# Optimization experiments

Measured on AMD Instinct MI355X. Metric: run time of the kernel, lower is better.

The kernel has to match this reference:

```python
import jax, jax.numpy as jnp
import numpy as np

N = 50000   # nodes
E = 600000  # edges per relation
H = 4       # heads
DH = 32     # head dim (out_feat // num_heads)
D = 128     # in_feat == out_feat
NEG_SLOPE = 0.2


def setup_inputs() -> dict:
    key = jax.random.key(0)
    ks = jax.random.split(key, 13)
    x = jax.random.normal(ks[0], (N, D), jnp.float32)
    src_r0 = jax.random.randint(ks[1], (E,), 0, N, jnp.int32)
    dst_r0 = jax.random.randint(ks[2], (E,), 0, N, jnp.int32)
    src_r1 = jax.random.randint(ks[3], (E,), 0, N, jnp.int32)
    dst_r1 = jax.random.randint(ks[4], (E,), 0, N, jnp.int32)
    s = 0.05  # keep activations moderate (xavier-like scale)
    W_r0 = jax.random.normal(ks[5], (D, H * DH), jnp.float32) * s
    attn_l_r0 = jax.random.normal(ks[6], (H, DH), jnp.float32) * s
    attn_r_r0 = jax.random.normal(ks[7], (H, DH), jnp.float32) * s
    W_r1 = jax.random.normal(ks[8], (D, H * DH), jnp.float32) * s
    attn_l_r1 = jax.random.normal(ks[9], (H, DH), jnp.float32) * s
    attn_r_r1 = jax.random.normal(ks[10], (H, DH), jnp.float32) * s
    loop_weight = jax.random.normal(ks[11], (D, D), jnp.float32) * s
    h_bias = jnp.zeros((D,), jnp.float32)
    return {"x": x, "src_r0": src_r0, "dst_r0": dst_r0, "src_r1": src_r1,
            "dst_r1": dst_r1, "W_r0": W_r0, "attn_l_r0": attn_l_r0,
            "attn_r_r0": attn_r_r0, "W_r1": W_r1, "attn_l_r1": attn_l_r1,
            "attn_r_r1": attn_r_r1, "loop_weight": loop_weight, "h_bias": h_bias}


def _gat_rel(x, src, dst, W, attn_l, attn_r):
    """DGL GATConv for one relation: fc -> per-node attn scalars -> edge
    leaky_relu -> per-dst softmax -> weighted scatter-sum. Heads flattened."""
    feat = (x @ W).reshape(-1, H, DH)                 # [N, H, DH]
    el = jnp.einsum('nhd,hd->nh', feat, attn_l)       # [N, H]
    er = jnp.einsum('nhd,hd->nh', feat, attn_r)       # [N, H]
    e = jax.nn.leaky_relu(el[src] + er[dst], NEG_SLOPE)  # [E, H]
    # edge softmax per destination node, per head (numerically stable)
    m = jax.ops.segment_max(e, dst, num_segments=N)   # [N, H]
    ex = jnp.exp(e - m[dst])                          # [E, H]
    z = jax.ops.segment_sum(ex, dst, num_segments=N)  # [N, H]
    a = ex / z[dst]                                   # [E, H]
    msg = a[:, :, None] * feat[src]                   # [E, H, DH]
    out = jax.ops.segment_sum(msg, dst, num_segments=N)  # [N, H, DH]
    return out.reshape(-1, H * DH)                    # [N, D] (concat heads)


def reference(x, src_r0, dst_r0, src_r1, dst_r1, W_r0, attn_l_r0, attn_r_r0,
              W_r1, attn_l_r1, attn_r_r1, loop_weight, h_bias):
    # HeteroGraphConv with default 'sum' aggregation across relations
    h = _gat_rel(x, src_r0, dst_r0, W_r0, attn_l_r0, attn_r_r0)
    h = h + _gat_rel(x, src_r1, dst_r1, W_r1, attn_l_r1, attn_r_r1)
    # self-loop linear + bias + activation (dropout p=0.0 is identity)
    h = h + x @ loop_weight + h_bias
    return jax.nn.relu(h)
```

## Files before the change

kernel.cpp:

```cpp
#include <hip/hip_runtime.h>
#include <math.h>


#define CAP 48
#define NB 256
#define BCAP 2752
#define BIN_EDGES 4096

typedef __attribute__((ext_vector_type(8))) short short8v;
typedef __attribute__((ext_vector_type(4))) float float4v;

__device__ __forceinline__ unsigned short f2bf(float f) {
  unsigned int u = __float_as_uint(f);
  unsigned int r = (u + 0x7fffu + ((u >> 16) & 1u)) >> 16;
  return (unsigned short)r;
}
__device__ __forceinline__ float2 bfpair(unsigned int u) {
  float2 r;
  r.x = __uint_as_float(u << 16);
  r.y = __uint_as_float(u & 0xffff0000u);
  return r;
}

__global__ __launch_bounds__(512) void prep_bin_kernel(
    const float* __restrict__ W0, const float* __restrict__ W1,
    const float* __restrict__ WL,
    const float* __restrict__ al0, const float* __restrict__ ar0,
    const float* __restrict__ al1, const float* __restrict__ ar1,
    const int* __restrict__ src0, const int* __restrict__ dst0,
    const int* __restrict__ src1, const int* __restrict__ dst1,
    unsigned short* __restrict__ Wtall,
    unsigned int* __restrict__ bpair, int* __restrict__ gcnt,
    int E, int width, int nconvb, int nbin)
{
  __shared__ int smem[512];
  const int t = threadIdx.x;

  if ((int)blockIdx.x < nconvb) {
    const int j = blockIdx.x * 512 + t;
    if (j < 4096) {
      const int rel = j >> 11;
      const int q = j & 2047;
      const int n = q >> 4;
      const int k0 = (q & 15) * 8;
      const float* W = rel ? W1 : W0;
      unsigned short o[8];
#pragma unroll
      for (int u = 0; u < 8; ++u) o[u] = f2bf(W[(size_t)(k0 + u) * 128 + n]);
      *(short8v*)&Wtall[(size_t)rel * 18432 + n * 128 + k0] = *(short8v*)o;
    } else if (j < 4352) {
      const int e = j - 4096;
      const int rel = e >> 7;
      const int q = e & 127;
      const int cIdx = q >> 4;
      const int isr = cIdx >> 2;
      const int h = cIdx & 3;
      const int k0 = (q & 15) * 8;
      const float* W = rel ? W1 : W0;
      const float* av = isr ? (rel ? ar1 : ar0) : (rel ? al1 : al0);
      unsigned short o[8];
#pragma unroll
      for (int u = 0; u < 8; ++u) {
        float s = 0.f;
#pragma unroll
        for (int d = 0; d < 32; ++d)
          s += W[(size_t)(k0 + u) * 128 + h * 32 + d] * av[h * 32 + d];
        o[u] = f2bf(s);
      }
      *(short8v*)&Wtall[(size_t)rel * 18432 + (128 + cIdx) * 128 + k0] = *(short8v*)o;
    } else if (j < 4608) {
      const int e = j - 4352;
      const int rel = e >> 7;
      const int q = e & 127;
      const int cIdx = 136 + (q >> 4);
      const int k0 = (q & 15) * 8;
      const short8v z = {0,0,0,0,0,0,0,0};
      *(short8v*)&Wtall[(size_t)rel * 18432 + cIdx * 128 + k0] = z;
    } else if (j < 6656) {
      const int e = j - 4608;
      const int n = e >> 4;
      const int k0 = (e & 15) * 8;
      unsigned short o[8];
#pragma unroll
      for (int u = 0; u < 8; ++u) o[u] = f2bf(WL[(size_t)(k0 + u) * 128 + n]);
      *(short8v*)&Wtall[(size_t)2 * 18432 + n * 128 + k0] = *(short8v*)o;
    }
  } else {
    int* cnt = smem;
    int* gb  = smem + NB;
    const int bid = blockIdx.x - nconvb;
    const int rel = (bid >= nbin) ? 1 : 0;
    const int ib  = rel ? (bid - nbin) : bid;
    const int* srcA = rel ? src1 : src0;
    const int* dstA = rel ? dst1 : dst0;
    const int base = ib * BIN_EDGES;
    const int cntE = min(E - base, BIN_EDGES);

    for (int i = t; i < NB; i += 512) cnt[i] = 0;
    __syncthreads();

    unsigned int epack[8]; int eb[8], epos[8];
#pragma unroll
    for (int q = 0; q < 8; ++q) {
      const int ei = t * 8 + q;
      if (ei < cntE) {
        const int s = srcA[base + ei];
        const int d = dstA[base + ei];
        const int b = d / width;
        const int ld = d - b * width;
        epack[q] = (unsigned int)s | ((unsigned int)ld << 16);
        eb[q] = b;
        epos[q] = atomicAdd(&cnt[b], 1);
      } else {
        eb[q] = -1;
      }
    }
    __syncthreads();
    for (int i = t; i < NB; i += 512)
      gb[i] = atomicAdd(&gcnt[rel * NB + i], cnt[i]);
    __syncthreads();
#pragma unroll
    for (int q = 0; q < 8; ++q) {
      if (eb[q] >= 0) {
        const int slot = gb[eb[q]] + epos[q];
        if (slot < BCAP)
          bpair[(size_t)(rel * NB + eb[q]) * BCAP + slot] = epack[q];
      }
    }
  }
}

__global__ __launch_bounds__(256) void gemm_ell_kernel(
    const float* __restrict__ x, const unsigned short* __restrict__ Wtall,
    unsigned short* __restrict__ f0, unsigned short* __restrict__ f1,
    unsigned short* __restrict__ xl,
    float* __restrict__ el0, float* __restrict__ er0,
    float* __restrict__ el1, float* __restrict__ er1,
    const unsigned int* __restrict__ bpair, const int* __restrict__ gcnt,
    int* __restrict__ deg, unsigned short* __restrict__ ell0,
    unsigned short* __restrict__ ell1,
    int N, int width, int ngemm)
{
  __shared__ int ldeg[256];

  if ((int)blockIdx.x < ngemm) {
    const int wave = threadIdx.x >> 6, lane = threadIdx.x & 63;
    const int lr = lane & 15, lk = lane >> 4;
    const int row0 = blockIdx.x * 64 + wave * 16;
    const int r = row0 + lr;

    short8v a[4];
#pragma unroll
    for (int kc = 0; kc < 4; ++kc) {
      if (r < N) {
        const float* xp = &x[(size_t)r * 128 + kc * 32 + lk * 8];
        float4 u = *(const float4*)xp;
        float4 v = *(const float4*)(xp + 4);
        unsigned short o[8];
        o[0]=f2bf(u.x); o[1]=f2bf(u.y); o[2]=f2bf(u.z); o[3]=f2bf(u.w);
        o[4]=f2bf(v.x); o[5]=f2bf(v.y); o[6]=f2bf(v.z); o[7]=f2bf(v.w);
        a[kc] = *(short8v*)o;
      } else {
        a[kc] = (short8v){0,0,0,0,0,0,0,0};
      }
    }

#pragma unroll
    for (int w = 0; w < 3; ++w) {
      const unsigned short* Wp = Wtall + (size_t)w * 18432;
      const int NF = (w < 2) ? 9 : 8;
      float4v acc[9];
#pragma unroll
      for (int nf = 0; nf < 9; ++nf) acc[nf] = (float4v){0.f, 0.f, 0.f, 0.f};
      for (int nf = 0; nf < NF; ++nf) {
        const unsigned short* Bp = &Wp[(size_t)(nf * 16 + lr) * 128];
#pragma unroll
        for (int kc = 0; kc < 4; ++kc) {
          const short8v b = *(const short8v*)&Bp[kc * 32 + lk * 8];
          acc[nf] = __builtin_amdgcn_mfma_f32_16x16x32_bf16(a[kc], b, acc[nf], 0, 0, 0);
        }
      }

      unsigned short* dstp = (w == 0) ? f0 : (w == 1) ? f1 : xl;
#pragma unroll
      for (int nf = 0; nf < 8; ++nf) {
        const int col = nf * 16 + lr;
#pragma unroll
        for (int j = 0; j < 4; ++j) {
          const int row = row0 + lk * 4 + j;
          if (row < N) dstp[(size_t)row * 128 + col] = f2bf(acc[nf][j]);
        }
      }
      if (w < 2 && lr < 8) {
        float* ep = (lr < 4) ? (w ? el1 : el0) : (w ? er1 : er0);
        const int h = lr & 3;
#pragma unroll
        for (int j = 0; j < 4; ++j) {
          const int row = row0 + lk * 4 + j;
          if (row < N) ep[row * 4 + h] = acc[8][j];
        }
      }
    }
  } else {
    const int bid = blockIdx.x - ngemm;
    const int rel = bid >> 8;
    const int b = bid & 255;
    const int t = threadIdx.x;
    const int d0 = b * width;
    if (t < width) ldeg[t] = 0;
    __syncthreads();
    const int count = min(gcnt[rel * NB + b], BCAP);
    unsigned short* ell = rel ? ell1 : ell0;
    const unsigned int* bp = &bpair[(size_t)(rel * NB + b) * BCAP];
    for (int i = t; i < count; i += 256) {
      const unsigned int v = bp[i];
      const int src = (int)(v & 0xFFFFu);
      const int ld = (int)(v >> 16);
      const int slot = atomicAdd(&ldeg[ld], 1);
      if (slot < CAP) ell[(size_t)(d0 + ld) * CAP + slot] = (unsigned short)src;
    }
    __syncthreads();
    if (t < width && d0 + t < N) deg[rel * N + d0 + t] = ldeg[t];
  }
}

__global__ __launch_bounds__(256) void gat_aggregate_kernel(
    const unsigned short* __restrict__ f0, const unsigned short* __restrict__ f1,
    const unsigned short* __restrict__ xl,
    const float* __restrict__ el0, const float* __restrict__ er0,
    const float* __restrict__ el1, const float* __restrict__ er1,
    const int* __restrict__ deg,
    const unsigned short* __restrict__ ell0, const unsigned short* __restrict__ ell1,
    const float* __restrict__ bias, float* __restrict__ out, int N)
{
  __shared__ float p_lds[4][2][4][16];
  const int wid  = threadIdx.x >> 6;
  const int lane = threadIdx.x & 63;
  const int n = blockIdx.x * 4 + wid;
  if (n >= N) return;
  const int h  = lane >> 4;
  const int il = lane & 15;
  const int c  = lane * 2;

  const int rs0 = (int)ell0[(size_t)n * CAP + il];
  const int rs1 = (int)ell1[(size_t)n * CAP + il];
  const int d0 = min(deg[n], CAP);
  const int d1 = min(deg[N + n], CAP);
  const float er0h = er0[n * 4 + h];
  const float er1h = er1[n * 4 + h];

  const bool v0 = il < d0, v1 = il < d1;
  const int s0 = v0 ? rs0 : 0;
  const int s1 = v1 ? rs1 : 0;
  const float elv0 = el0[s0 * 4 + h];
  const float elv1 = el1[s1 * 4 + h];

  float m0, sum0, m1, sum1;
  {
    float e = elv0 + er0h;  e = e > 0.f ? e : 0.2f * e;
    float ev = v0 ? e : -INFINITY;
    float cm = ev;
    cm = fmaxf(cm, __shfl_xor(cm, 1)); cm = fmaxf(cm, __shfl_xor(cm, 2));
    cm = fmaxf(cm, __shfl_xor(cm, 4)); cm = fmaxf(cm, __shfl_xor(cm, 8));
    const float p = __expf(ev - cm);
    float cs = p;
    cs += __shfl_xor(cs, 1); cs += __shfl_xor(cs, 2);
    cs += __shfl_xor(cs, 4); cs += __shfl_xor(cs, 8);
    m0 = cm; sum0 = cs;
    p_lds[wid][0][h][il] = p;
  }
  {
    float e = elv1 + er1h;  e = e > 0.f ? e : 0.2f * e;
    float ev = v1 ? e : -INFINITY;
    float cm = ev;
    cm = fmaxf(cm, __shfl_xor(cm, 1)); cm = fmaxf(cm, __shfl_xor(cm, 2));
    cm = fmaxf(cm, __shfl_xor(cm, 4)); cm = fmaxf(cm, __shfl_xor(cm, 8));
    const float p = __expf(ev - cm);
    float cs = p;
    cs += __shfl_xor(cs, 1); cs += __shfl_xor(cs, 2);
    cs += __shfl_xor(cs, 4); cs += __shfl_xor(cs, 8);
    m1 = cm; sum1 = cs;
    p_lds[wid][1][h][il] = p;
  }

  unsigned int fu0[16], fu1[16];
#pragma unroll
  for (int i = 0; i < 16; ++i) {
    const int s = __builtin_amdgcn_readlane(s0, i);
    fu0[i] = *(const unsigned int*)&f0[(size_t)s * 128 + c];
  }
#pragma unroll
  for (int i = 0; i < 16; ++i) {
    const int s = __builtin_amdgcn_readlane(s1, i);
    fu1[i] = *(const unsigned int*)&f1[(size_t)s * 128 + c];
  }

  float ax0 = 0.f, ay0 = 0.f;
  {
    float p16[16];
    *(float4*)&p16[0]  = *(const float4*)&p_lds[wid][0][h][0];
    *(float4*)&p16[4]  = *(const float4*)&p_lds[wid][0][h][4];
    *(float4*)&p16[8]  = *(const float4*)&p_lds[wid][0][h][8];
    *(float4*)&p16[12] = *(const float4*)&p_lds[wid][0][h][12];
    float axa=0.f, aya=0.f, axb=0.f, ayb=0.f;
#pragma unroll
    for (int i = 0; i < 16; i += 2) {
      const float2 fa = bfpair(fu0[i]);
      const float2 fb2 = bfpair(fu0[i+1]);
      axa += p16[i]*fa.x;   aya += p16[i]*fa.y;
      axb += p16[i+1]*fb2.x; ayb += p16[i+1]*fb2.y;
    }
    ax0 = axa + axb; ay0 = aya + ayb;
  }
  float ax1 = 0.f, ay1 = 0.f;
  {
    float p16[16];
    *(float4*)&p16[0]  = *(const float4*)&p_lds[wid][1][h][0];
    *(float4*)&p16[4]  = *(const float4*)&p_lds[wid][1][h][4];
    *(float4*)&p16[8]  = *(const float4*)&p_lds[wid][1][h][8];
    *(float4*)&p16[12] = *(const float4*)&p_lds[wid][1][h][12];
    float axa=0.f, aya=0.f, axb=0.f, ayb=0.f;
#pragma unroll
    for (int i = 0; i < 16; i += 2) {
      const float2 fa = bfpair(fu1[i]);
      const float2 fb2 = bfpair(fu1[i+1]);
      axa += p16[i]*fa.x;   aya += p16[i]*fa.y;
      axb += p16[i+1]*fb2.x; ayb += p16[i+1]*fb2.y;
    }
    ax1 = axa + axb; ay1 = aya + ayb;
  }

  auto tail = [&](const unsigned short* ellp, const float* elp, float erh,
                  int d, const unsigned short* fbp, float& m, float& sum,
                  float& ax, float& ay, int slot) {
    for (int base = 16; base < d; base += 16) {
      const bool valid = (base + il) < d;
      int sv = (int)ellp[(size_t)n * CAP + base + il];
      sv = valid ? sv : 0;
      const float elv = elp[sv * 4 + h];
      float e = elv + erh; e = e > 0.f ? e : 0.2f * e;
      const float ev = valid ? e : -INFINITY;
      float cm = ev;
      cm = fmaxf(cm, __shfl_xor(cm, 1)); cm = fmaxf(cm, __shfl_xor(cm, 2));
      cm = fmaxf(cm, __shfl_xor(cm, 4)); cm = fmaxf(cm, __shfl_xor(cm, 8));
      const float mn = fmaxf(m, cm);
      const float scale = __expf(m - mn);
      const float p = __expf(ev - mn);
      float cs = p;
      cs += __shfl_xor(cs, 1); cs += __shfl_xor(cs, 2);
      cs += __shfl_xor(cs, 4); cs += __shfl_xor(cs, 8);
      sum = sum * scale + cs;
      m = mn;
      p_lds[wid][slot][h][il] = p;
      unsigned int fu[16];
#pragma unroll
      for (int i = 0; i < 16; ++i) {
        const int s = __builtin_amdgcn_readlane(sv, i);
        fu[i] = *(const unsigned int*)&fbp[(size_t)s * 128 + c];
      }
      float p16[16];
      *(float4*)&p16[0]  = *(const float4*)&p_lds[wid][slot][h][0];
      *(float4*)&p16[4]  = *(const float4*)&p_lds[wid][slot][h][4];
      *(float4*)&p16[8]  = *(const float4*)&p_lds[wid][slot][h][8];
      *(float4*)&p16[12] = *(const float4*)&p_lds[wid][slot][h][12];
      float axa=0.f, aya=0.f;
#pragma unroll
      for (int i = 0; i < 16; ++i) {
        const float2 f = bfpair(fu[i]);
        axa += p16[i]*f.x; aya += p16[i]*f.y;
      }
      ax = ax * scale + axa;
      ay = ay * scale + aya;
    }
  };
  if (d0 > 16) tail(ell0, el0, er0h, d0, f0, m0, sum0, ax0, ay0, 0);
  if (d1 > 16) tail(ell1, el1, er1h, d1, f1, m1, sum1, ax1, ay1, 1);

  float ox = 0.f, oy = 0.f;
  if (d0 > 0) { const float inv = 1.f / sum0; ox += ax0 * inv; oy += ay0 * inv; }
  if (d1 > 0) { const float inv = 1.f / sum1; ox += ax1 * inv; oy += ay1 * inv; }
  const float2 xlv = bfpair(*(const unsigned int*)&xl[(size_t)n * 128 + c]);
  const float2 bv  = *(const float2*)&bias[c];
  ox += xlv.x + bv.x;
  oy += xlv.y + bv.y;
  float2 res;
  res.x = fmaxf(ox, 0.f);
  res.y = fmaxf(oy, 0.f);
  *(float2*)&out[(size_t)n * 128 + c] = res;
}

extern "C" void kernel_launch(void* const* d_in, const int* in_sizes, int n_in,
                              void* d_out, int out_size, void* d_ws, size_t ws_size,
                              hipStream_t stream)
{
  const int N = in_sizes[0] / 128;
  const int E = in_sizes[1];

  const float* x    = (const float*)d_in[0];
  const int* src0   = (const int*)d_in[1];
  const int* dst0   = (const int*)d_in[2];
  const int* src1   = (const int*)d_in[3];
  const int* dst1   = (const int*)d_in[4];
  const float* W0   = (const float*)d_in[5];
  const float* al0  = (const float*)d_in[6];
  const float* ar0  = (const float*)d_in[7];
  const float* W1   = (const float*)d_in[8];
  const float* al1  = (const float*)d_in[9];
  const float* ar1  = (const float*)d_in[10];
  const float* WL   = (const float*)d_in[11];
  const float* bias = (const float*)d_in[12];
  float* out = (float*)d_out;

  char* p = (char*)d_ws;
  auto alloc = [&](size_t bytes) { char* r = p; p += (bytes + 255) & ~(size_t)255; return r; };
  unsigned short* f0 = (unsigned short*)alloc((size_t)N * 128 * 2);
  unsigned short* f1 = (unsigned short*)alloc((size_t)N * 128 * 2);
  unsigned short* xl = (unsigned short*)alloc((size_t)N * 128 * 2);
  float* el0 = (float*)alloc((size_t)N * 4 * 4);
  float* er0 = (float*)alloc((size_t)N * 4 * 4);
  float* el1 = (float*)alloc((size_t)N * 4 * 4);
  float* er1 = (float*)alloc((size_t)N * 4 * 4);
  int* deg   = (int*)alloc((size_t)2 * N * 4);
  unsigned short* ell0 = (unsigned short*)alloc((size_t)CAP * N * 2);
  unsigned short* ell1 = (unsigned short*)alloc((size_t)CAP * N * 2);
  unsigned int* bpair = (unsigned int*)alloc((size_t)2 * NB * BCAP * 4);
  int* gcnt  = (int*)alloc((size_t)2 * NB * 4);
  unsigned short* Wtall = (unsigned short*)alloc((size_t)(2 * 144 + 128) * 128 * 2);

  const int width = (N + NB - 1) / NB;
  const int ngemm = (N + 63) / 64;
  const int nbin  = (E + BIN_EDGES - 1) / BIN_EDGES;
  const int nconvb = 13;

  hipMemsetAsync(gcnt, 0, (size_t)2 * NB * 4, stream);

  prep_bin_kernel<<<nconvb + 2 * nbin, 512, 0, stream>>>(
      W0, W1, WL, al0, ar0, al1, ar1, src0, dst0, src1, dst1,
      Wtall, bpair, gcnt, E, width, nconvb, nbin);

  gemm_ell_kernel<<<ngemm + 2 * NB, 256, 0, stream>>>(
      x, Wtall, f0, f1, xl, el0, er0, el1, er1,
      bpair, gcnt, deg, ell0, ell1, N, width, ngemm);

  gat_aggregate_kernel<<<(N + 3) / 4, 256, 0, stream>>>(
      f0, f1, xl, el0, er0, el1, er1, deg, ell0, ell1, bias, out, N);
}
```

Measured before the change: 153.4 us.

## Process more work per thread across binning, GEMM, and aggregation kernels

The binning stage now handles 8192 edges per block, with 16 edges per thread in a strided coalesced layout. The GEMM computes two 16-row M fragments per wave, so each B-fragment load feeds two MFMAs. The aggregation kernel processes two destination nodes per wave so more independent gathers are in flight. The cost is higher register pressure and fewer blocks, which may reduce occupancy.

```diff
diff --git a/kernel.cpp b/kernel.cpp
--- a/kernel.cpp
+++ b/kernel.cpp
@@ -5,7 +5,7 @@
 #define CAP 48
 #define NB 256
 #define BCAP 2752
-#define BIN_EDGES 4096
+#define BIN_EDGES 8192
 
 typedef __attribute__((ext_vector_type(8))) short short8v;
 typedef __attribute__((ext_vector_type(4))) float float4v;
@@ -99,10 +99,10 @@
     for (int i = t; i < NB; i += 512) cnt[i] = 0;
     __syncthreads();
 
-    unsigned int epack[8]; int eb[8], epos[8];
-#pragma unroll
-    for (int q = 0; q < 8; ++q) {
-      const int ei = t * 8 + q;
+    unsigned int epack[16]; int eb[16], epos[16];
+#pragma unroll
+    for (int q = 0; q < 16; ++q) {
+      const int ei = q * 512 + t;
       if (ei < cntE) {
         const int s = srcA[base + ei];
         const int d = dstA[base + ei];
@@ -120,7 +120,7 @@
       gb[i] = atomicAdd(&gcnt[rel * NB + i], cnt[i]);
     __syncthreads();
 #pragma unroll
-    for (int q = 0; q < 8; ++q) {
+    for (int q = 0; q < 16; ++q) {
       if (eb[q] >= 0) {
         const int slot = gb[eb[q]] + epos[q];
         if (slot < BCAP)
@@ -146,22 +146,25 @@
   if ((int)blockIdx.x < ngemm) {
     const int wave = threadIdx.x >> 6, lane = threadIdx.x & 63;
     const int lr = lane & 15, lk = lane >> 4;
-    const int row0 = blockIdx.x * 64 + wave * 16;
-    const int r = row0 + lr;
-
-    short8v a[4];
-#pragma unroll
-    for (int kc = 0; kc < 4; ++kc) {
-      if (r < N) {
-        const float* xp = &x[(size_t)r * 128 + kc * 32 + lk * 8];
-        float4 u = *(const float4*)xp;
-        float4 v = *(const float4*)(xp + 4);
-        unsigned short o[8];
-        o[0]=f2bf(u.x); o[1]=f2bf(u.y); o[2]=f2bf(u.z); o[3]=f2bf(u.w);
-        o[4]=f2bf(v.x); o[5]=f2bf(v.y); o[6]=f2bf(v.z); o[7]=f2bf(v.w);
-        a[kc] = *(short8v*)o;
-      } else {
-        a[kc] = (short8v){0,0,0,0,0,0,0,0};
+    const int row0 = blockIdx.x * 128 + wave * 32;
+
+    short8v a[2][4];
+#pragma unroll
+    for (int mf = 0; mf < 2; ++mf) {
+      const int r = row0 + mf * 16 + lr;
+#pragma unroll
+      for (int kc = 0; kc < 4; ++kc) {
+        if (r < N) {
+          const float* xp = &x[(size_t)r * 128 + kc * 32 + lk * 8];
+          float4 u = *(const float4*)xp;
+          float4 v = *(const float4*)(xp + 4);
+          unsigned short o[8];
+          o[0]=f2bf(u.x); o[1]=f2bf(u.y); o[2]=f2bf(u.z); o[3]=f2bf(u.w);
+          o[4]=f2bf(v.x); o[5]=f2bf(v.y); o[6]=f2bf(v.z); o[7]=f2bf(v.w);
+          a[mf][kc] = *(short8v*)o;
+        } else {
+          a[mf][kc] = (short8v){0,0,0,0,0,0,0,0};
+        }
       }
     }
 
@@ -169,36 +172,44 @@
     for (int w = 0; w < 3; ++w) {
       const unsigned short* Wp = Wtall + (size_t)w * 18432;
       const int NF = (w < 2) ? 9 : 8;
-      float4v acc[9];
-#pragma unroll
-      for (int nf = 0; nf < 9; ++nf) acc[nf] = (float4v){0.f, 0.f, 0.f, 0.f};
+      float4v acc[2][9];
+#pragma unroll
+      for (int mf = 0; mf < 2; ++mf)
+#pragma unroll
+        for (int nf = 0; nf < 9; ++nf) acc[mf][nf] = (float4v){0.f, 0.f, 0.f, 0.f};
       for (int nf = 0; nf < NF; ++nf) {
         const unsigned short* Bp = &Wp[(size_t)(nf * 16 + lr) * 128];
 #pragma unroll
         for (int kc = 0; kc < 4; ++kc) {
           const short8v b = *(const short8v*)&Bp[kc * 32 + lk * 8];
-          acc[nf] = __builtin_amdgcn_mfma_f32_16x16x32_bf16(a[kc], b, acc[nf], 0, 0, 0);
+          acc[0][nf] = __builtin_amdgcn_mfma_f32_16x16x32_bf16(a[0][kc], b, acc[0][nf], 0, 0, 0);
+          acc[1][nf] = __builtin_amdgcn_mfma_f32_16x16x32_bf16(a[1][kc], b, acc[1][nf], 0, 0, 0);
         }
       }
 
       unsigned short* dstp = (w == 0) ? f0 : (w == 1) ? f1 : xl;
 #pragma unroll
-      for (int nf = 0; nf < 8; ++nf) {
-        const int col = nf * 16 + lr;
-#pragma unroll
-        for (int j = 0; j < 4; ++j) {
-          const int row = row0 + lk * 4 + j;
-          if (row < N) dstp[(size_t)row * 128 + col] = f2bf(acc[nf][j]);
+      for (int mf = 0; mf < 2; ++mf) {
+#pragma unroll
+        for (int nf = 0; nf < 8; ++nf) {
+          const int col = nf * 16 + lr;
+#pragma unroll
+          for (int j = 0; j < 4; ++j) {
+            const int row = row0 + mf * 16 + lk * 4 + j;
+            if (row < N) dstp[(size_t)row * 128 + col] = f2bf(acc[mf][nf][j]);
+          }
         }
       }
       if (w < 2 && lr < 8) {
         float* ep = (lr < 4) ? (w ? el1 : el0) : (w ? er1 : er0);
         const int h = lr & 3;
 #pragma unroll
-        for (int j = 0; j < 4; ++j) {
-          const int row = row0 + lk * 4 + j;
-          if (row < N) ep[row * 4 + h] = acc[8][j];
-        }
+        for (int mf = 0; mf < 2; ++mf)
+#pragma unroll
+          for (int j = 0; j < 4; ++j) {
+            const int row = row0 + mf * 16 + lk * 4 + j;
+            if (row < N) ep[row * 4 + h] = acc[mf][8][j];
+          }
       }
     }
   } else {
@@ -233,112 +244,110 @@
     const unsigned short* __restrict__ ell0, const unsigned short* __restrict__ ell1,
     const float* __restrict__ bias, float* __restrict__ out, int N)
 {
-  __shared__ float p_lds[4][2][4][16];
+  __shared__ float p_lds[4][2][2][4][16];
   const int wid  = threadIdx.x >> 6;
   const int lane = threadIdx.x & 63;
-  const int n = blockIdx.x * 4 + wid;
-  if (n >= N) return;
   const int h  = lane >> 4;
   const int il = lane & 15;
   const int c  = lane * 2;
-
-  const int rs0 = (int)ell0[(size_t)n * CAP + il];
-  const int rs1 = (int)ell1[(size_t)n * CAP + il];
-  const int d0 = min(deg[n], CAP);
-  const int d1 = min(deg[N + n], CAP);
-  const float er0h = er0[n * 4 + h];
-  const float er1h = er1[n * 4 + h];
-
-  const bool v0 = il < d0, v1 = il < d1;
-  const int s0 = v0 ? rs0 : 0;
-  const int s1 = v1 ? rs1 : 0;
-  const float elv0 = el0[s0 * 4 + h];
-  const float elv1 = el1[s1 * 4 + h];
-
-  float m0, sum0, m1, sum1;
-  {
-    float e = elv0 + er0h;  e = e > 0.f ? e : 0.2f * e;
-    float ev = v0 ? e : -INFINITY;
-    float cm = ev;
-    cm = fmaxf(cm, __shfl_xor(cm, 1)); cm = fmaxf(cm, __shfl_xor(cm, 2));
-    cm = fmaxf(cm, __shfl_xor(cm, 4)); cm = fmaxf(cm, __shfl_xor(cm, 8));
-    const float p = __expf(ev - cm);
-    float cs = p;
-    cs += __shfl_xor(cs, 1); cs += __shfl_xor(cs, 2);
-    cs += __shfl_xor(cs, 4); cs += __shfl_xor(cs, 8);
-    m0 = cm; sum0 = cs;
-    p_lds[wid][0][h][il] = p;
-  }
-  {
-    float e = elv1 + er1h;  e = e > 0.f ? e : 0.2f * e;
-    float ev = v1 ? e : -INFINITY;
-    float cm = ev;
-    cm = fmaxf(cm, __shfl_xor(cm, 1)); cm = fmaxf(cm, __shfl_xor(cm, 2));
-    cm = fmaxf(cm, __shfl_xor(cm, 4)); cm = fmaxf(cm, __shfl_xor(cm, 8));
-    const float p = __expf(ev - cm);
-    float cs = p;
-    cs += __shfl_xor(cs, 1); cs += __shfl_xor(cs, 2);
-    cs += __shfl_xor(cs, 4); cs += __shfl_xor(cs, 8);
-    m1 = cm; sum1 = cs;
-    p_lds[wid][1][h][il] = p;
-  }
-
-  unsigned int fu0[16], fu1[16];
-#pragma unroll
-  for (int i = 0; i < 16; ++i) {
-    const int s = __builtin_amdgcn_readlane(s0, i);
-    fu0[i] = *(const unsigned int*)&f0[(size_t)s * 128 + c];
-  }
-#pragma unroll
-  for (int i = 0; i < 16; ++i) {
-    const int s = __builtin_amdgcn_readlane(s1, i);
-    fu1[i] = *(const unsigned int*)&f1[(size_t)s * 128 + c];
-  }
-
-  float ax0 = 0.f, ay0 = 0.f;
-  {
-    float p16[16];
-    *(float4*)&p16[0]  = *(const float4*)&p_lds[wid][0][h][0];
-    *(float4*)&p16[4]  = *(const float4*)&p_lds[wid][0][h][4];
-    *(float4*)&p16[8]  = *(const float4*)&p_lds[wid][0][h][8];
-    *(float4*)&p16[12] = *(const float4*)&p_lds[wid][0][h][12];
-    float axa=0.f, aya=0.f, axb=0.f, ayb=0.f;
-#pragma unroll
-    for (int i = 0; i < 16; i += 2) {
-      const float2 fa = bfpair(fu0[i]);
-      const float2 fb2 = bfpair(fu0[i+1]);
-      axa += p16[i]*fa.x;   aya += p16[i]*fa.y;
-      axb += p16[i+1]*fb2.x; ayb += p16[i+1]*fb2.y;
-    }
-    ax0 = axa + axb; ay0 = aya + ayb;
-  }
-  float ax1 = 0.f, ay1 = 0.f;
-  {
-    float p16[16];
-    *(float4*)&p16[0]  = *(const float4*)&p_lds[wid][1][h][0];
-    *(float4*)&p16[4]  = *(const float4*)&p_lds[wid][1][h][4];
-    *(float4*)&p16[8]  = *(const float4*)&p_lds[wid][1][h][8];
-    *(float4*)&p16[12] = *(const float4*)&p_lds[wid][1][h][12];
-    float axa=0.f, aya=0.f, axb=0.f, ayb=0.f;
-#pragma unroll
-    for (int i = 0; i < 16; i += 2) {
-      const float2 fa = bfpair(fu1[i]);
-      const float2 fb2 = bfpair(fu1[i+1]);
-      axa += p16[i]*fa.x;   aya += p16[i]*fa.y;
-      axb += p16[i+1]*fb2.x; ayb += p16[i+1]*fb2.y;
-    }
-    ax1 = axa + axb; ay1 = aya + ayb;
-  }
-
-  auto tail = [&](const unsigned short* ellp, const float* elp, float erh,
+  const int nraw = blockIdx.x * 8 + wid * 2;
+
+  int nn[2]; bool act[2];
+#pragma unroll
+  for (int q = 0; q < 2; ++q) {
+    const int nr = nraw + q;
+    act[q] = nr < N;
+    nn[q] = act[q] ? nr : (N - 1);
+  }
+
+  int ss[2][2], dd[2][2];
+  float erh[2][2];
+#pragma unroll
+  for (int q = 0; q < 2; ++q) {
+    const int n = nn[q];
+    const int r0 = (int)ell0[(size_t)n * CAP + il];
+    const int r1 = (int)ell1[(size_t)n * CAP + il];
+    dd[q][0] = act[q] ? min(deg[n], CAP) : 0;
+    dd[q][1] = act[q] ? min(deg[N + n], CAP) : 0;
+    erh[q][0] = er0[n * 4 + h];
+    erh[q][1] = er1[n * 4 + h];
+    ss[q][0] = (il < dd[q][0]) ? r0 : 0;
+    ss[q][1] = (il < dd[q][1]) ? r1 : 0;
+  }
+
+  float elv[2][2];
+#pragma unroll
+  for (int q = 0; q < 2; ++q) {
+    elv[q][0] = el0[ss[q][0] * 4 + h];
+    elv[q][1] = el1[ss[q][1] * 4 + h];
+  }
+
+  float mm[2][2], su[2][2];
+#pragma unroll
+  for (int q = 0; q < 2; ++q) {
+#pragma unroll
+    for (int rel = 0; rel < 2; ++rel) {
+      float e = elv[q][rel] + erh[q][rel];
+      e = e > 0.f ? e : 0.2f * e;
+      const float ev = (il < dd[q][rel]) ? e : -INFINITY;
+      float cm = ev;
+      cm = fmaxf(cm, __shfl_xor(cm, 1)); cm = fmaxf(cm, __shfl_xor(cm, 2));
+      cm = fmaxf(cm, __shfl_xor(cm, 4)); cm = fmaxf(cm, __shfl_xor(cm, 8));
+      const float p = __expf(ev - cm);
+      float cs = p;
+      cs += __shfl_xor(cs, 1); cs += __shfl_xor(cs, 2);
+      cs += __shfl_xor(cs, 4); cs += __shfl_xor(cs, 8);
+      mm[q][rel] = cm; su[q][rel] = cs;
+      p_lds[wid][q][rel][h][il] = p;
+    }
+  }
+
+  unsigned int fu[2][2][16];
+#pragma unroll
+  for (int q = 0; q < 2; ++q) {
+#pragma unroll
+    for (int i = 0; i < 16; ++i) {
+      const int s = __builtin_amdgcn_readlane(ss[q][0], i);
+      fu[q][0][i] = *(const unsigned int*)&f0[(size_t)s * 128 + c];
+    }
+#pragma unroll
+    for (int i = 0; i < 16; ++i) {
+      const int s = __builtin_amdgcn_readlane(ss[q][1], i);
+      fu[q][1][i] = *(const unsigned int*)&f1[(size_t)s * 128 + c];
+    }
+  }
+
+  float ax[2][2], ay[2][2];
+#pragma unroll
+  for (int q = 0; q < 2; ++q) {
+#pragma unroll
+    for (int rel = 0; rel < 2; ++rel) {
+      float p16[16];
+      *(float4*)&p16[0]  = *(const float4*)&p_lds[wid][q][rel][h][0];
+      *(float4*)&p16[4]  = *(const float4*)&p_lds[wid][q][rel][h][4];
+      *(float4*)&p16[8]  = *(const float4*)&p_lds[wid][q][rel][h][8];
+      *(float4*)&p16[12] = *(const float4*)&p_lds[wid][q][rel][h][12];
+      float axa=0.f, aya=0.f, axb=0.f, ayb=0.f;
+#pragma unroll
+      for (int i = 0; i < 16; i += 2) {
+        const float2 fa = bfpair(fu[q][rel][i]);
+        const float2 fb2 = bfpair(fu[q][rel][i+1]);
+        axa += p16[i]*fa.x;   aya += p16[i]*fa.y;
+        axb += p16[i+1]*fb2.x; ayb += p16[i+1]*fb2.y;
+      }
+      ax[q][rel] = axa + axb; ay[q][rel] = aya + ayb;
+    }
+  }
+
+  auto tail = [&](int n, const unsigned short* ellp, const float* elp, float erhv,
                   int d, const unsigned short* fbp, float& m, float& sum,
-                  float& ax, float& ay, int slot) {
+                  float& axr, float& ayr, int q, int rel) {
     for (int base = 16; base < d; base += 16) {
       const bool valid = (base + il) < d;
       int sv = (int)ellp[(size_t)n * CAP + base + il];
       sv = valid ? sv : 0;
-      const float elv = elp[sv * 4 + h];
-      float e = elv + erh; e = e > 0.f ? e : 0.2f * e;
+      const float elvv = elp[sv * 4 + h];
+      float e = elvv + erhv; e = e > 0.f ? e : 0.2f * e;
       const float ev = valid ? e : -INFINITY;
       float cm = ev;
       cm = fmaxf(cm, __shfl_xor(cm, 1)); cm = fmaxf(cm, __shfl_xor(cm, 2));
@@ -351,42 +360,49 @@
       cs += __shfl_xor(cs, 4); cs += __shfl_xor(cs, 8);
       sum = sum * scale + cs;
       m = mn;
-      p_lds[wid][slot][h][il] = p;
-      unsigned int fu[16];
+      p_lds[wid][q][rel][h][il] = p;
+      unsigned int fuv[16];
 #pragma unroll
       for (int i = 0; i < 16; ++i) {
         const int s = __builtin_amdgcn_readlane(sv, i);
-        fu[i] = *(const unsigned int*)&fbp[(size_t)s * 128 + c];
+        fuv[i] = *(const unsigned int*)&fbp[(size_t)s * 128 + c];
       }
       float p16[16];
-      *(float4*)&p16[0]  = *(const float4*)&p_lds[wid][slot][h][0];
-      *(float4*)&p16[4]  = *(const float4*)&p_lds[wid][slot][h][4];
-      *(float4*)&p16[8]  = *(const float4*)&p_lds[wid][slot][h][8];
-      *(float4*)&p16[12] = *(const float4*)&p_lds[wid][slot][h][12];
+      *(float4*)&p16[0]  = *(const float4*)&p_lds[wid][q][rel][h][0];
+      *(float4*)&p16[4]  = *(const float4*)&p_lds[wid][q][rel][h][4];
+      *(float4*)&p16[8]  = *(const float4*)&p_lds[wid][q][rel][h][8];
+      *(float4*)&p16[12] = *(const float4*)&p_lds[wid][q][rel][h][12];
       float axa=0.f, aya=0.f;
 #pragma unroll
       for (int i = 0; i < 16; ++i) {
-        const float2 f = bfpair(fu[i]);
+        const float2 f = bfpair(fuv[i]);
         axa += p16[i]*f.x; aya += p16[i]*f.y;
       }
-      ax = ax * scale + axa;
-      ay = ay * scale + aya;
+      axr = axr * scale + axa;
+      ayr = ayr * scale + aya;
     }
   };
-  if (d0 > 16) tail(ell0, el0, er0h, d0, f0, m0, sum0, ax0, ay0, 0);
-  if (d1 > 16) tail(ell1, el1, er1h, d1, f1, m1, sum1, ax1, ay1, 1);
-
-  float ox = 0.f, oy = 0.f;
-  if (d0 > 0) { const float inv = 1.f / sum0; ox += ax0 * inv; oy += ay0 * inv; }
-  if (d1 > 0) { const float inv = 1.f / sum1; ox += ax1 * inv; oy += ay1 * inv; }
-  const float2 xlv = bfpair(*(const unsigned int*)&xl[(size_t)n * 128 + c]);
-  const float2 bv  = *(const float2*)&bias[c];
-  ox += xlv.x + bv.x;
-  oy += xlv.y + bv.y;
-  float2 res;
-  res.x = fmaxf(ox, 0.f);
-  res.y = fmaxf(oy, 0.f);
-  *(float2*)&out[(size_t)n * 128 + c] = res;
+  if (dd[0][0] > 16) tail(nn[0], ell0, el0, erh[0][0], dd[0][0], f0, mm[0][0], su[0][0], ax[0][0], ay[0][0], 0, 0);
+  if (dd[0][1] > 16) tail(nn[0], ell1, el1, erh[0][1], dd[0][1], f1, mm[0][1], su[0][1], ax[0][1], ay[0][1], 0, 1);
+  if (dd[1][0] > 16) tail(nn[1], ell0, el0, erh[1][0], dd[1][0], f0, mm[1][0], su[1][0], ax[1][0], ay[1][0], 1, 0);
+  if (dd[1][1] > 16) tail(nn[1], ell1, el1, erh[1][1], dd[1][1], f1, mm[1][1], su[1][1], ax[1][1], ay[1][1], 1, 1);
+
+#pragma unroll
+  for (int q = 0; q < 2; ++q) {
+    if (!act[q]) continue;
+    const int n = nn[q];
+    float ox = 0.f, oy = 0.f;
+    if (dd[q][0] > 0) { const float inv = 1.f / su[q][0]; ox += ax[q][0] * inv; oy += ay[q][0] * inv; }
+    if (dd[q][1] > 0) { const float inv = 1.f / su[q][1]; ox += ax[q][1] * inv; oy += ay[q][1] * inv; }
+    const float2 xlv = bfpair(*(const unsigned int*)&xl[(size_t)n * 128 + c]);
+    const float2 bv  = *(const float2*)&bias[c];
+    ox += xlv.x + bv.x;
+    oy += xlv.y + bv.y;
+    float2 res;
+    res.x = fmaxf(ox, 0.f);
+    res.y = fmaxf(oy, 0.f);
+    *(float2*)&out[(size_t)n * 128 + c] = res;
+  }
 }
 
 extern "C" void kernel_launch(void* const* d_in, const int* in_sizes, int n_in,
@@ -428,7 +444,7 @@
   unsigned short* Wtall = (unsigned short*)alloc((size_t)(2 * 144 + 128) * 128 * 2);
 
   const int width = (N + NB - 1) / NB;
-  const int ngemm = (N + 63) / 64;
+  const int ngemm = (N + 127) / 128;
   const int nbin  = (E + BIN_EDGES - 1) / BIN_EDGES;
   const int nconvb = 13;
 
@@ -442,6 +458,6 @@
       x, Wtall, f0, f1, xl, el0, er0, el1, er1,
       bpair, gcnt, deg, ell0, ell1, N, width, ngemm);
 
-  gat_aggregate_kernel<<<(N + 3) / 4, 256, 0, stream>>>(
+  gat_aggregate_kernel<<<(N + 7) / 8, 256, 0, stream>>>(
       f0, f1, xl, el0, er0, el1, er1, deg, ell0, ell1, bias, out, N);
 }
```

Measured after the change: 156.3 us. No clear change (+1.9%).

## Double GEMM rows per wave and enlarge edge-binning chunks with coalesced loads

Applied to the files above, without the earlier changes.

Each GEMM wave now computes two 16-row M fragments that share every loaded B (weight) fragment, so each block covers 128 rows and the grid halves, cutting redundant weight reads. The binning blocks now process 8192 edges with 16 edges per thread and use strided indexing (q*512+t), which makes the src/dst loads coalesced. This also halves the number of global atomics on the bin counters. The trade-off is higher register pressure (18 accumulators) and fewer blocks, which could lower occupancy and parallelism.

```diff
diff --git a/kernel.cpp b/kernel.cpp
--- a/kernel.cpp
+++ b/kernel.cpp
@@ -5,7 +5,7 @@
 #define CAP 48
 #define NB 256
 #define BCAP 2752
-#define BIN_EDGES 4096
+#define BIN_EDGES 8192
 
 typedef __attribute__((ext_vector_type(8))) short short8v;
 typedef __attribute__((ext_vector_type(4))) float float4v;
@@ -99,10 +99,10 @@
     for (int i = t; i < NB; i += 512) cnt[i] = 0;
     __syncthreads();
 
-    unsigned int epack[8]; int eb[8], epos[8];
-#pragma unroll
-    for (int q = 0; q < 8; ++q) {
-      const int ei = t * 8 + q;
+    unsigned int epack[16]; int eb[16], epos[16];
+#pragma unroll
+    for (int q = 0; q < 16; ++q) {
+      const int ei = q * 512 + t;
       if (ei < cntE) {
         const int s = srcA[base + ei];
         const int d = dstA[base + ei];
@@ -120,7 +120,7 @@
       gb[i] = atomicAdd(&gcnt[rel * NB + i], cnt[i]);
     __syncthreads();
 #pragma unroll
-    for (int q = 0; q < 8; ++q) {
+    for (int q = 0; q < 16; ++q) {
       if (eb[q] >= 0) {
         const int slot = gb[eb[q]] + epos[q];
         if (slot < BCAP)
@@ -146,22 +146,25 @@
   if ((int)blockIdx.x < ngemm) {
     const int wave = threadIdx.x >> 6, lane = threadIdx.x & 63;
     const int lr = lane & 15, lk = lane >> 4;
-    const int row0 = blockIdx.x * 64 + wave * 16;
-    const int r = row0 + lr;
-
-    short8v a[4];
-#pragma unroll
-    for (int kc = 0; kc < 4; ++kc) {
-      if (r < N) {
-        const float* xp = &x[(size_t)r * 128 + kc * 32 + lk * 8];
-        float4 u = *(const float4*)xp;
-        float4 v = *(const float4*)(xp + 4);
-        unsigned short o[8];
-        o[0]=f2bf(u.x); o[1]=f2bf(u.y); o[2]=f2bf(u.z); o[3]=f2bf(u.w);
-        o[4]=f2bf(v.x); o[5]=f2bf(v.y); o[6]=f2bf(v.z); o[7]=f2bf(v.w);
-        a[kc] = *(short8v*)o;
-      } else {
-        a[kc] = (short8v){0,0,0,0,0,0,0,0};
+    const int row0 = blockIdx.x * 128 + wave * 32;
+
+    short8v a[2][4];
+#pragma unroll
+    for (int mf = 0; mf < 2; ++mf) {
+      const int r = row0 + mf * 16 + lr;
+#pragma unroll
+      for (int kc = 0; kc < 4; ++kc) {
+        if (r < N) {
+          const float* xp = &x[(size_t)r * 128 + kc * 32 + lk * 8];
+          float4 u = *(const float4*)xp;
+          float4 v = *(const float4*)(xp + 4);
+          unsigned short o[8];
+          o[0]=f2bf(u.x); o[1]=f2bf(u.y); o[2]=f2bf(u.z); o[3]=f2bf(u.w);
+          o[4]=f2bf(v.x); o[5]=f2bf(v.y); o[6]=f2bf(v.z); o[7]=f2bf(v.w);
+          a[mf][kc] = *(short8v*)o;
+        } else {
+          a[mf][kc] = (short8v){0,0,0,0,0,0,0,0};
+        }
       }
     }
 
@@ -169,36 +172,44 @@
     for (int w = 0; w < 3; ++w) {
       const unsigned short* Wp = Wtall + (size_t)w * 18432;
       const int NF = (w < 2) ? 9 : 8;
-      float4v acc[9];
-#pragma unroll
-      for (int nf = 0; nf < 9; ++nf) acc[nf] = (float4v){0.f, 0.f, 0.f, 0.f};
+      float4v acc[2][9];
+#pragma unroll
+      for (int mf = 0; mf < 2; ++mf)
+#pragma unroll
+        for (int nf = 0; nf < 9; ++nf) acc[mf][nf] = (float4v){0.f, 0.f, 0.f, 0.f};
       for (int nf = 0; nf < NF; ++nf) {
         const unsigned short* Bp = &Wp[(size_t)(nf * 16 + lr) * 128];
 #pragma unroll
         for (int kc = 0; kc < 4; ++kc) {
           const short8v b = *(const short8v*)&Bp[kc * 32 + lk * 8];
-          acc[nf] = __builtin_amdgcn_mfma_f32_16x16x32_bf16(a[kc], b, acc[nf], 0, 0, 0);
+          acc[0][nf] = __builtin_amdgcn_mfma_f32_16x16x32_bf16(a[0][kc], b, acc[0][nf], 0, 0, 0);
+          acc[1][nf] = __builtin_amdgcn_mfma_f32_16x16x32_bf16(a[1][kc], b, acc[1][nf], 0, 0, 0);
         }
       }
 
       unsigned short* dstp = (w == 0) ? f0 : (w == 1) ? f1 : xl;
 #pragma unroll
-      for (int nf = 0; nf < 8; ++nf) {
-        const int col = nf * 16 + lr;
-#pragma unroll
-        for (int j = 0; j < 4; ++j) {
-          const int row = row0 + lk * 4 + j;
-          if (row < N) dstp[(size_t)row * 128 + col] = f2bf(acc[nf][j]);
+      for (int mf = 0; mf < 2; ++mf) {
+#pragma unroll
+        for (int nf = 0; nf < 8; ++nf) {
+          const int col = nf * 16 + lr;
+#pragma unroll
+          for (int j = 0; j < 4; ++j) {
+            const int row = row0 + mf * 16 + lk * 4 + j;
+            if (row < N) dstp[(size_t)row * 128 + col] = f2bf(acc[mf][nf][j]);
+          }
         }
       }
       if (w < 2 && lr < 8) {
         float* ep = (lr < 4) ? (w ? el1 : el0) : (w ? er1 : er0);
         const int h = lr & 3;
 #pragma unroll
-        for (int j = 0; j < 4; ++j) {
-          const int row = row0 + lk * 4 + j;
-          if (row < N) ep[row * 4 + h] = acc[8][j];
-        }
+        for (int mf = 0; mf < 2; ++mf)
+#pragma unroll
+          for (int j = 0; j < 4; ++j) {
+            const int row = row0 + mf * 16 + lk * 4 + j;
+            if (row < N) ep[row * 4 + h] = acc[mf][8][j];
+          }
       }
     }
   } else {
@@ -428,7 +439,7 @@
   unsigned short* Wtall = (unsigned short*)alloc((size_t)(2 * 144 + 128) * 128 * 2);
 
   const int width = (N + NB - 1) / NB;
-  const int ngemm = (N + 63) / 64;
+  const int ngemm = (N + 127) / 128;
   const int nbin  = (E + BIN_EDGES - 1) / BIN_EDGES;
   const int nconvb = 13;
 
```

Result: faster. 128.9 us (-16.0%).
